# Kernel optimization log

Hardware: AMD Instinct MI355X
Metric: run time of the kernel (lower is better)

The kernel has to match this reference:

```python
import jax, jax.numpy as jnp
import numpy as np

N, B, E = 10000, 4, 160000
C_IN, C_OUT, C_E = 64, 64, 16


def _mk_params(key, c_in, c_out, c_e):
    ks = jax.random.split(key, 8)
    s = 0.1
    return dict(
        w_n=jax.random.normal(ks[0], (c_in, c_out), jnp.float32) * s,
        w_e=jax.random.normal(ks[1], (c_e, c_out), jnp.float32) * s,
        q=jax.random.normal(ks[2], (c_out, c_out), jnp.float32) * s,
        k=jax.random.normal(ks[3], (c_out, c_out), jnp.float32) * s,
        aw=jax.random.normal(ks[4], (3 * c_out, 1), jnp.float32) * s,
        ab=jax.random.normal(ks[5], (1,), jnp.float32) * s,
        ow=jax.random.normal(ks[6], (2 * c_out, c_out), jnp.float32) * s,
        ob=jax.random.normal(ks[7], (c_out,), jnp.float32) * s,
    )


def setup_inputs() -> dict:
    key = jax.random.key(0)
    kx, ke, ka, k1, k2 = jax.random.split(key, 5)
    inp = {
        'X': jax.random.normal(kx, (N, B, C_IN), jnp.float32),
        'edge_index': jax.random.randint(ke, (2, E), 0, N, jnp.int32),
        'edge_attr': jax.random.normal(ka, (E, C_E), jnp.float32),
    }
    p1 = _mk_params(k1, C_IN, C_OUT, C_E)
    p2 = _mk_params(k2, C_OUT, C_OUT, C_E)
    for name, v in p1.items():
        inp[name + '1'] = v
    for name, v in p2.items():
        inp[name + '2'] = v
    return inp


def egnn_conv(x, edge_index, edge_attr, w_n, w_e, q, k, aw, ab, ow, ob, n_nodes):
    # x: [N,B,Cin]; edge_attr: [E,Ce]
    xp = x @ w_n                         # [N,B,C]
    ea = edge_attr @ w_e                 # [E,C]
    src, dst = edge_index[0], edge_index[1]
    xj = xp[src]                         # [E,B,C] gather (source)
    xi = xp[dst]                         # [E,B,C] gather (target)
    qf = xj @ q                          # [E,B,C]
    kf = xi @ k                          # [E,B,C]
    eab = jnp.broadcast_to(ea[:, None, :], qf.shape)  # [E,B,C]
    att_feat = jnp.concatenate([qf, kf, eab], axis=-1)  # [E,B,3C]
    att = jax.nn.sigmoid(att_feat @ aw + ab)            # [E,B,1]
    gate = jax.nn.sigmoid(eab)
    msg = att * xj * gate                # [E,B,C]
    aggr = jax.ops.segment_max(msg, dst, num_segments=n_nodes)  # [N,B,C]
    aggr = jnp.where(jnp.isneginf(aggr), 0.0, aggr)  # empty segments -> 0
    out = jnp.concatenate([xp, aggr], axis=-1) @ ow + ob
    return xp + out


def reference(X, edge_index, edge_attr,
              w_n1, w_e1, q1, k1, aw1, ab1, ow1, ob1,
              w_n2, w_e2, q2, k2, aw2, ab2, ow2, ob2):
    n_nodes = X.shape[0]
    c1 = egnn_conv(X, edge_index, edge_attr, w_n1, w_e1, q1, k1, aw1, ab1, ow1, ob1, n_nodes)
    c1 = jax.nn.leaky_relu(c1, 0.01)
    c2 = egnn_conv(c1, edge_index, edge_attr, w_n2, w_e2, q2, k2, aw2, ab2, ow2, ob2, n_nodes)
    c2 = jax.nn.leaky_relu(c2, 0.01)
    return c2
```

## Files before the change

kernel.cpp:

```cpp
#include <hip/hip_runtime.h>
#include <math.h>

#define NN 10000
#define BB 4
#define EE 160000
#define CC 64
#define CE 16

static constexpr size_t OFF_XPA    = 0;
static constexpr size_t OFF_XPB    = 10240000;
static constexpr size_t OFF_SA     = 20480000;
static constexpr size_t OFF_SB     = 20640000;
static constexpr size_t OFF_VECS   = 20800000;
static constexpr size_t OFF_COUNTS = 20801280;
static constexpr size_t OFF_CURSOR = 20841280;
static constexpr size_t OFF_OFFS   = 20881280;
static constexpr size_t OFF_RECS   = 20921344;
static constexpr size_t OFF_ATT    = 22201344;
static constexpr size_t OFF_SE12   = 24761344;
static constexpr size_t OFF_ORDER  = 26041344;

__device__ __forceinline__ float sigmoidf_(float x) {
    return __builtin_amdgcn_rcpf(1.0f + __expf(-x));
}

__global__ void hist_vecs_kernel(const int* __restrict__ ei, int* __restrict__ counts,
                                 const float* __restrict__ q1, const float* __restrict__ k1,
                                 const float* __restrict__ aw1, const float* __restrict__ we1,
                                 const float* __restrict__ q2, const float* __restrict__ k2,
                                 const float* __restrict__ aw2, const float* __restrict__ we2,
                                 float* __restrict__ vecs) {
    int e = blockIdx.x * blockDim.x + threadIdx.x;
    if (e < EE) atomicAdd(&counts[ei[EE + e]], 1);
    if (blockIdx.x == 0) {
        int t = threadIdx.x;
        if (t < 64) {
            float a = 0.f, b = 0.f, c = 0.f, d = 0.f;
            for (int j = 0; j < 64; ++j) {
                a = fmaf(q1[t * 64 + j], aw1[j], a);
                b = fmaf(k1[t * 64 + j], aw1[64 + j], b);
                c = fmaf(q2[t * 64 + j], aw2[j], c);
                d = fmaf(k2[t * 64 + j], aw2[64 + j], d);
            }
            vecs[t] = a; vecs[64 + t] = b; vecs[144 + t] = c; vecs[208 + t] = d;
        }
        if (t < 16) {
            float a = 0.f, b = 0.f;
            for (int j = 0; j < 64; ++j) {
                a = fmaf(we1[t * 64 + j], aw1[128 + j], a);
                b = fmaf(we2[t * 64 + j], aw2[128 + j], b);
            }
            vecs[128 + t] = a; vecs[272 + t] = b;
        }
    }
}

__global__ __launch_bounds__(1024) void scan_kernel(const int* __restrict__ counts,
                                                    int* __restrict__ offs, int n) {
    __shared__ int wsum[16];
    int t = threadIdx.x;
    int base = t * 10;
    int v[10];
    int s = 0;
    #pragma unroll
    for (int j = 0; j < 10; ++j) {
        int i = base + j;
        v[j] = (i < n) ? counts[i] : 0;
        s += v[j];
    }
    int lane = t & 63, wid = t >> 6;
    int ps = s;
    #pragma unroll
    for (int off = 1; off < 64; off <<= 1) {
        int u = __shfl_up(ps, off, 64);
        if (lane >= off) ps += u;
    }
    if (lane == 63) wsum[wid] = ps;
    __syncthreads();
    int wbase = 0;
    for (int w = 0; w < wid; ++w) wbase += wsum[w];
    int tb = wbase + ps - s;
    #pragma unroll
    for (int j = 0; j < 10; ++j) {
        int i = base + j;
        if (i < n) offs[i] = tb;
        tb += v[j];
    }
    if (t == 1023) offs[n] = tb;
}

__global__ __launch_bounds__(1024) void order_kernel(const int* __restrict__ counts,
                                                     int* __restrict__ order) {
    __shared__ int hist[1024];
    __shared__ int startb[1024];
    __shared__ int cur[1024];
    __shared__ int wsum[16];
    int t = threadIdx.x;
    hist[t] = 0; cur[t] = 0;
    __syncthreads();
    int dg[10];
    #pragma unroll
    for (int j = 0; j < 10; ++j) {
        int i = t * 10 + j;
        dg[j] = -1;
        if (i < NN) {
            int d = counts[i];
            d = (d > 1023) ? 1023 : d;
            dg[j] = d;
            atomicAdd(&hist[d], 1);
        }
    }
    __syncthreads();
    int r = 1023 - t;
    int v = hist[r];
    int lane = t & 63, wid = t >> 6;
    int ps = v;
    #pragma unroll
    for (int off = 1; off < 64; off <<= 1) {
        int u = __shfl_up(ps, off, 64);
        if (lane >= off) ps += u;
    }
    if (lane == 63) wsum[wid] = ps;
    __syncthreads();
    int wbase = 0;
    for (int w = 0; w < wid; ++w) wbase += wsum[w];
    startb[r] = wbase + ps - v;
    __syncthreads();
    #pragma unroll
    for (int j = 0; j < 10; ++j) {
        if (dg[j] >= 0) {
            int pos = startb[dg[j]] + atomicAdd(&cur[dg[j]], 1);
            order[pos] = t * 10 + j;
        }
    }
}

__global__ __launch_bounds__(256) void scatter_kernel(
    const int* __restrict__ ei, const int* __restrict__ offs,
    int* __restrict__ cursor, const float* __restrict__ attr,
    const float* __restrict__ vecs, const float* __restrict__ ab1,
    const float* __restrict__ ab2, int2* __restrict__ recs,
    float2* __restrict__ se12) {
    int e = blockIdx.x * blockDim.x + threadIdx.x;
    if (e >= EE) return;
    int s = ei[e], d = ei[EE + e];
    const float4* ap = (const float4*)(attr + (size_t)e * CE);
    float4 a0 = ap[0], a1 = ap[1], a2 = ap[2], a3 = ap[3];
    const float* v1 = vecs + 128;
    const float* v2 = vecs + 272;
    float s1 = ab1[0], s2 = ab2[0];
    s1 = fmaf(a0.x, v1[0], s1);  s1 = fmaf(a0.y, v1[1], s1);
    s1 = fmaf(a0.z, v1[2], s1);  s1 = fmaf(a0.w, v1[3], s1);
    s1 = fmaf(a1.x, v1[4], s1);  s1 = fmaf(a1.y, v1[5], s1);
    s1 = fmaf(a1.z, v1[6], s1);  s1 = fmaf(a1.w, v1[7], s1);
    s1 = fmaf(a2.x, v1[8], s1);  s1 = fmaf(a2.y, v1[9], s1);
    s1 = fmaf(a2.z, v1[10], s1); s1 = fmaf(a2.w, v1[11], s1);
    s1 = fmaf(a3.x, v1[12], s1); s1 = fmaf(a3.y, v1[13], s1);
    s1 = fmaf(a3.z, v1[14], s1); s1 = fmaf(a3.w, v1[15], s1);
    s2 = fmaf(a0.x, v2[0], s2);  s2 = fmaf(a0.y, v2[1], s2);
    s2 = fmaf(a0.z, v2[2], s2);  s2 = fmaf(a0.w, v2[3], s2);
    s2 = fmaf(a1.x, v2[4], s2);  s2 = fmaf(a1.y, v2[5], s2);
    s2 = fmaf(a1.z, v2[6], s2);  s2 = fmaf(a1.w, v2[7], s2);
    s2 = fmaf(a2.x, v2[8], s2);  s2 = fmaf(a2.y, v2[9], s2);
    s2 = fmaf(a2.z, v2[10], s2); s2 = fmaf(a2.w, v2[11], s2);
    s2 = fmaf(a3.x, v2[12], s2); s2 = fmaf(a3.y, v2[13], s2);
    s2 = fmaf(a3.z, v2[14], s2); s2 = fmaf(a3.w, v2[15], s2);
    int p = atomicAdd(&cursor[d], 1);
    recs[offs[d] + p] = make_int2(s, e);
    se12[e] = make_float2(s1, s2);
}

__global__ __launch_bounds__(256) void node_prep_kernel(
    const float* __restrict__ x,
    const float* __restrict__ w_n,
    const float* __restrict__ qa,
    const float* __restrict__ ka,
    float* __restrict__ xp,
    float* __restrict__ sa,
    float* __restrict__ sb) {
    __shared__ float w_sh[64 * 64];
    __shared__ float x_sh[4 * BB * CC];
    int t = threadIdx.x;
    for (int i = t; i < 64 * 64; i += 256) w_sh[i] = w_n[i];
    int node0 = blockIdx.x * 4;
    const float4* xg = (const float4*)(x + (size_t)node0 * BB * CC);
    ((float4*)x_sh)[t] = xg[t];
    __syncthreads();
    int wave = t >> 6, lane = t & 63;
    int node = node0 + wave;
    const float* xrow = x_sh + wave * BB * CC;
    float acc0 = 0.f, acc1 = 0.f, acc2 = 0.f, acc3 = 0.f;
    #pragma unroll 8
    for (int ci = 0; ci < 64; ++ci) {
        float w = w_sh[ci * 64 + lane];
        acc0 = fmaf(xrow[ci], w, acc0);
        acc1 = fmaf(xrow[64 + ci], w, acc1);
        acc2 = fmaf(xrow[128 + ci], w, acc2);
        acc3 = fmaf(xrow[192 + ci], w, acc3);
    }
    size_t obase = (size_t)node * BB * CC + lane;
    xp[obase] = acc0;
    xp[obase + 64] = acc1;
    xp[obase + 128] = acc2;
    xp[obase + 192] = acc3;
    float qv = qa[lane], kv = ka[lane];
    float ra0 = acc0 * qv, ra1 = acc1 * qv, ra2 = acc2 * qv, ra3 = acc3 * qv;
    float rb0 = acc0 * kv, rb1 = acc1 * kv, rb2 = acc2 * kv, rb3 = acc3 * kv;
    #pragma unroll
    for (int off = 32; off >= 1; off >>= 1) {
        ra0 += __shfl_xor(ra0, off, 64); ra1 += __shfl_xor(ra1, off, 64);
        ra2 += __shfl_xor(ra2, off, 64); ra3 += __shfl_xor(ra3, off, 64);
        rb0 += __shfl_xor(rb0, off, 64); rb1 += __shfl_xor(rb1, off, 64);
        rb2 += __shfl_xor(rb2, off, 64); rb3 += __shfl_xor(rb3, off, 64);
    }
    if (lane == 0) {
        sa[node * BB + 0] = ra0; sa[node * BB + 1] = ra1;
        sa[node * BB + 2] = ra2; sa[node * BB + 3] = ra3;
        sb[node * BB + 0] = rb0; sb[node * BB + 1] = rb1;
        sb[node * BB + 2] = rb2; sb[node * BB + 3] = rb3;
    }
}

__global__ __launch_bounds__(256) void att_kernel(
    const int* __restrict__ ei, const float2* __restrict__ se12,
    const float* __restrict__ sa, const float* __restrict__ sb,
    float4* __restrict__ att, int sel) {
    int e = blockIdx.x * blockDim.x + threadIdx.x;
    if (e >= EE) return;
    int s = ei[e], d = ei[EE + e];
    float2 se2 = se12[e];
    float se = sel ? se2.y : se2.x;
    float4 sas = *(const float4*)(sa + (size_t)s * BB);
    float4 sbn = *(const float4*)(sb + (size_t)d * BB);
    float4 r;
    r.x = sigmoidf_(sas.x + sbn.x + se);
    r.y = sigmoidf_(sas.y + sbn.y + se);
    r.z = sigmoidf_(sas.z + sbn.z + se);
    r.w = sigmoidf_(sas.w + sbn.w + se);
    att[e] = r;
}

__global__ __launch_bounds__(256) void conv_out_kernel(
    const float* __restrict__ xp,
    const int2* __restrict__ recs,
    const int* __restrict__ offs,
    const float* __restrict__ attr,
    const float* __restrict__ w_e,
    const float4* __restrict__ att,
    const float* __restrict__ ow,
    const float* __restrict__ ob,
    const int* __restrict__ order,
    float* __restrict__ out) {
    __shared__ float aggr_sh[4][BB * CC];
    __shared__ float xpn_sh[4][BB * CC];
    int t = threadIdx.x;
    int wave = t >> 6, lane = t & 63;
    int node = order[blockIdx.x * 4 + wave];

    float wec[CE];
    #pragma unroll
    for (int j = 0; j < CE; ++j) wec[j] = w_e[j * CC + lane];

    const float* xn = xp + (size_t)node * BB * CC + lane;
    float xn0 = xn[0], xn1 = xn[64], xn2 = xn[128], xn3 = xn[192];

    int o0 = offs[node], o1 = offs[node + 1];
    float m0 = -INFINITY, m1 = -INFINITY, m2 = -INFINITY, m3 = -INFINITY;

    int i = o0;
    int2 rec = (i < o1) ? recs[i] : make_int2(0, 0);
    while (i < o1) {
        int2 cur = rec;
        ++i;
        if (i < o1) rec = recs[i];
        int s = cur.x, e = cur.y;
        float4 at = att[e];
        const float4* ap = (const float4*)(attr + (size_t)e * CE);
        float4 a0 = ap[0], a1 = ap[1], a2 = ap[2], a3 = ap[3];
        float g = 0.f;
        g = fmaf(a0.x, wec[0], g);  g = fmaf(a0.y, wec[1], g);
        g = fmaf(a0.z, wec[2], g);  g = fmaf(a0.w, wec[3], g);
        g = fmaf(a1.x, wec[4], g);  g = fmaf(a1.y, wec[5], g);
        g = fmaf(a1.z, wec[6], g);  g = fmaf(a1.w, wec[7], g);
        g = fmaf(a2.x, wec[8], g);  g = fmaf(a2.y, wec[9], g);
        g = fmaf(a2.z, wec[10], g); g = fmaf(a2.w, wec[11], g);
        g = fmaf(a3.x, wec[12], g); g = fmaf(a3.y, wec[13], g);
        g = fmaf(a3.z, wec[14], g); g = fmaf(a3.w, wec[15], g);
        g = sigmoidf_(g);
        const float* xs = xp + (size_t)s * BB * CC + lane;
        float x0 = xs[0], x1 = xs[64], x2 = xs[128], x3 = xs[192];
        m0 = fmaxf(m0, at.x * x0 * g);
        m1 = fmaxf(m1, at.y * x1 * g);
        m2 = fmaxf(m2, at.z * x2 * g);
        m3 = fmaxf(m3, at.w * x3 * g);
    }
    m0 = (m0 == -INFINITY) ? 0.f : m0;
    m1 = (m1 == -INFINITY) ? 0.f : m1;
    m2 = (m2 == -INFINITY) ? 0.f : m2;
    m3 = (m3 == -INFINITY) ? 0.f : m3;

    aggr_sh[wave][0 * CC + lane] = m0; aggr_sh[wave][1 * CC + lane] = m1;
    aggr_sh[wave][2 * CC + lane] = m2; aggr_sh[wave][3 * CC + lane] = m3;
    xpn_sh[wave][0 * CC + lane] = xn0; xpn_sh[wave][1 * CC + lane] = xn1;
    xpn_sh[wave][2 * CC + lane] = xn2; xpn_sh[wave][3 * CC + lane] = xn3;
    asm volatile("s_waitcnt lgkmcnt(0)" ::: "memory");

    const float* xr = xpn_sh[wave];
    const float* ar = aggr_sh[wave];
    float o0f = 0.f, o1f = 0.f, o2f = 0.f, o3f = 0.f;
    #pragma unroll 4
    for (int ci = 0; ci < 64; ++ci) {
        float wa = ow[ci * 64 + lane];
        float wb = ow[(64 + ci) * 64 + lane];
        o0f = fmaf(xr[ci], wa, o0f);
        o1f = fmaf(xr[CC + ci], wa, o1f);
        o2f = fmaf(xr[2 * CC + ci], wa, o2f);
        o3f = fmaf(xr[3 * CC + ci], wa, o3f);
        o0f = fmaf(ar[ci], wb, o0f);
        o1f = fmaf(ar[CC + ci], wb, o1f);
        o2f = fmaf(ar[2 * CC + ci], wb, o2f);
        o3f = fmaf(ar[3 * CC + ci], wb, o3f);
    }
    float obv = ob[lane];
    float r0 = xn0 + o0f + obv;
    float r1 = xn1 + o1f + obv;
    float r2 = xn2 + o2f + obv;
    float r3 = xn3 + o3f + obv;
    r0 = (r0 > 0.f) ? r0 : 0.01f * r0;
    r1 = (r1 > 0.f) ? r1 : 0.01f * r1;
    r2 = (r2 > 0.f) ? r2 : 0.01f * r2;
    r3 = (r3 > 0.f) ? r3 : 0.01f * r3;
    float* op = out + (size_t)node * BB * CC + lane;
    op[0] = r0; op[64] = r1; op[128] = r2; op[192] = r3;
}

extern "C" void kernel_launch(void* const* d_in, const int* in_sizes, int n_in,
                              void* d_out, int out_size, void* d_ws, size_t ws_size,
                              hipStream_t stream) {
    const float* X    = (const float*)d_in[0];
    const int*   ei   = (const int*)d_in[1];
    const float* attr = (const float*)d_in[2];
    const float* w_n1 = (const float*)d_in[3];
    const float* w_e1 = (const float*)d_in[4];
    const float* q1   = (const float*)d_in[5];
    const float* k1   = (const float*)d_in[6];
    const float* aw1  = (const float*)d_in[7];
    const float* ab1  = (const float*)d_in[8];
    const float* ow1  = (const float*)d_in[9];
    const float* ob1  = (const float*)d_in[10];
    const float* w_n2 = (const float*)d_in[11];
    const float* w_e2 = (const float*)d_in[12];
    const float* q2   = (const float*)d_in[13];
    const float* k2   = (const float*)d_in[14];
    const float* aw2  = (const float*)d_in[15];
    const float* ab2  = (const float*)d_in[16];
    const float* ow2  = (const float*)d_in[17];
    const float* ob2  = (const float*)d_in[18];
    float* out = (float*)d_out;

    char* ws = (char*)d_ws;
    float*  xpA    = (float*)(ws + OFF_XPA);
    float*  xpB    = (float*)(ws + OFF_XPB);
    float*  sa     = (float*)(ws + OFF_SA);
    float*  sb     = (float*)(ws + OFF_SB);
    float*  vecs   = (float*)(ws + OFF_VECS);
    int*    counts = (int*)(ws + OFF_COUNTS);
    int*    cursor = (int*)(ws + OFF_CURSOR);
    int*    offs   = (int*)(ws + OFF_OFFS);
    int2*   recs   = (int2*)(ws + OFF_RECS);
    float4* att    = (float4*)(ws + OFF_ATT);
    float2* se12   = (float2*)(ws + OFF_SE12);
    int*    order  = (int*)(ws + OFF_ORDER);

    hipMemsetAsync(counts, 0, 2 * NN * sizeof(int), stream);
    hist_vecs_kernel<<<EE / 256, 256, 0, stream>>>(ei, counts, q1, k1, aw1, w_e1,
                                                   q2, k2, aw2, w_e2, vecs);
    scan_kernel<<<1, 1024, 0, stream>>>(counts, offs, NN);
    order_kernel<<<1, 1024, 0, stream>>>(counts, order);
    scatter_kernel<<<EE / 256, 256, 0, stream>>>(ei, offs, cursor, attr, vecs,
                                                 ab1, ab2, recs, se12);
    node_prep_kernel<<<NN / 4, 256, 0, stream>>>(X, w_n1, vecs + 0, vecs + 64, xpA, sa, sb);
    att_kernel<<<EE / 256, 256, 0, stream>>>(ei, se12, sa, sb, att, 0);
    conv_out_kernel<<<NN / 4, 256, 0, stream>>>(xpA, recs, offs, attr, w_e1, att,
                                                ow1, ob1, order, xpB);
    node_prep_kernel<<<NN / 4, 256, 0, stream>>>(xpB, w_n2, vecs + 144, vecs + 208, xpA, sa, sb);
    att_kernel<<<EE / 256, 256, 0, stream>>>(ei, se12, sa, sb, att, 1);
    conv_out_kernel<<<NN / 4, 256, 0, stream>>>(xpA, recs, offs, attr, w_e2, att,
                                                ow2, ob2, order, out);
}
```

Before: 289.6 us.

## Merge scan and order kernels; vectorize conv_out output projection with float4 tiles

```diff
diff --git a/kernel.cpp b/kernel.cpp
--- a/kernel.cpp
+++ b/kernel.cpp
@@ -55,20 +55,24 @@
     }
 }
 
-__global__ __launch_bounds__(1024) void scan_kernel(const int* __restrict__ counts,
-                                                    int* __restrict__ offs, int n) {
+__global__ __launch_bounds__(1024) void scan_order_kernel(const int* __restrict__ counts,
+                                                          int* __restrict__ offs,
+                                                          int* __restrict__ order) {
+    __shared__ int hist[1024];
+    __shared__ int cur[1024];
+    __shared__ int startb[1024];
     __shared__ int wsum[16];
     int t = threadIdx.x;
-    int base = t * 10;
+    hist[t] = 0; cur[t] = 0;
+    int lane = t & 63, wid = t >> 6;
     int v[10];
     int s = 0;
     #pragma unroll
     for (int j = 0; j < 10; ++j) {
-        int i = base + j;
-        v[j] = (i < n) ? counts[i] : 0;
+        int i = t * 10 + j;
+        v[j] = (i < NN) ? counts[i] : 0;
         s += v[j];
     }
-    int lane = t & 63, wid = t >> 6;
     int ps = s;
     #pragma unroll
     for (int off = 1; off < 64; off <<= 1) {
@@ -82,55 +86,41 @@
     int tb = wbase + ps - s;
     #pragma unroll
     for (int j = 0; j < 10; ++j) {
-        int i = base + j;
-        if (i < n) offs[i] = tb;
+        int i = t * 10 + j;
+        if (i < NN) offs[i] = tb;
         tb += v[j];
     }
-    if (t == 1023) offs[n] = tb;
-}
-
-__global__ __launch_bounds__(1024) void order_kernel(const int* __restrict__ counts,
-                                                     int* __restrict__ order) {
-    __shared__ int hist[1024];
-    __shared__ int startb[1024];
-    __shared__ int cur[1024];
-    __shared__ int wsum[16];
-    int t = threadIdx.x;
-    hist[t] = 0; cur[t] = 0;
-    __syncthreads();
-    int dg[10];
+    if (t == 1023) offs[NN] = tb;
     #pragma unroll
     for (int j = 0; j < 10; ++j) {
         int i = t * 10 + j;
-        dg[j] = -1;
         if (i < NN) {
-            int d = counts[i];
-            d = (d > 1023) ? 1023 : d;
-            dg[j] = d;
+            int d = v[j] > 1023 ? 1023 : v[j];
             atomicAdd(&hist[d], 1);
         }
     }
     __syncthreads();
     int r = 1023 - t;
-    int v = hist[r];
-    int lane = t & 63, wid = t >> 6;
-    int ps = v;
+    int hv = hist[r];
+    int ps2 = hv;
     #pragma unroll
     for (int off = 1; off < 64; off <<= 1) {
-        int u = __shfl_up(ps, off, 64);
-        if (lane >= off) ps += u;
-    }
-    if (lane == 63) wsum[wid] = ps;
-    __syncthreads();
-    int wbase = 0;
-    for (int w = 0; w < wid; ++w) wbase += wsum[w];
-    startb[r] = wbase + ps - v;
+        int u = __shfl_up(ps2, off, 64);
+        if (lane >= off) ps2 += u;
+    }
+    if (lane == 63) wsum[wid] = ps2;
+    __syncthreads();
+    int wb2 = 0;
+    for (int w = 0; w < wid; ++w) wb2 += wsum[w];
+    startb[r] = wb2 + ps2 - hv;
     __syncthreads();
     #pragma unroll
     for (int j = 0; j < 10; ++j) {
-        if (dg[j] >= 0) {
-            int pos = startb[dg[j]] + atomicAdd(&cur[dg[j]], 1);
-            order[pos] = t * 10 + j;
+        int i = t * 10 + j;
+        if (i < NN) {
+            int d = v[j] > 1023 ? 1023 : v[j];
+            int pos = startb[d] + atomicAdd(&cur[d], 1);
+            order[pos] = i;
         }
     }
 }
@@ -171,13 +161,9 @@
 }
 
 __global__ __launch_bounds__(256) void node_prep_kernel(
-    const float* __restrict__ x,
-    const float* __restrict__ w_n,
-    const float* __restrict__ qa,
-    const float* __restrict__ ka,
-    float* __restrict__ xp,
-    float* __restrict__ sa,
-    float* __restrict__ sb) {
+    const float* __restrict__ x, const float* __restrict__ w_n,
+    const float* __restrict__ qa, const float* __restrict__ ka,
+    float* __restrict__ xp, float* __restrict__ sa, float* __restrict__ sb) {
     __shared__ float w_sh[64 * 64];
     __shared__ float x_sh[4 * BB * CC];
     int t = threadIdx.x;
@@ -240,6 +226,10 @@
     att[e] = r;
 }
 
+#define FMA4(o_, s_, w_)                                                 \
+    o_.x = fmaf(s_, w_.x, o_.x); o_.y = fmaf(s_, w_.y, o_.y);            \
+    o_.z = fmaf(s_, w_.z, o_.z); o_.w = fmaf(s_, w_.w, o_.w);
+
 __global__ __launch_bounds__(256) void conv_out_kernel(
     const float* __restrict__ xp,
     const int2* __restrict__ recs,
@@ -251,8 +241,7 @@
     const float* __restrict__ ob,
     const int* __restrict__ order,
     float* __restrict__ out) {
-    __shared__ float aggr_sh[4][BB * CC];
-    __shared__ float xpn_sh[4][BB * CC];
+    __shared__ float aggr_sh[4][BB * 68];
     int t = threadIdx.x;
     int wave = t >> 6, lane = t & 63;
     int node = order[blockIdx.x * 4 + wave];
@@ -260,9 +249,6 @@
     float wec[CE];
     #pragma unroll
     for (int j = 0; j < CE; ++j) wec[j] = w_e[j * CC + lane];
-
-    const float* xn = xp + (size_t)node * BB * CC + lane;
-    float xn0 = xn[0], xn1 = xn[64], xn2 = xn[128], xn3 = xn[192];
 
     int o0 = offs[node], o1 = offs[node + 1];
     float m0 = -INFINITY, m1 = -INFINITY, m2 = -INFINITY, m3 = -INFINITY;
@@ -299,39 +285,49 @@
     m2 = (m2 == -INFINITY) ? 0.f : m2;
     m3 = (m3 == -INFINITY) ? 0.f : m3;
 
-    aggr_sh[wave][0 * CC + lane] = m0; aggr_sh[wave][1 * CC + lane] = m1;
-    aggr_sh[wave][2 * CC + lane] = m2; aggr_sh[wave][3 * CC + lane] = m3;
-    xpn_sh[wave][0 * CC + lane] = xn0; xpn_sh[wave][1 * CC + lane] = xn1;
-    xpn_sh[wave][2 * CC + lane] = xn2; xpn_sh[wave][3 * CC + lane] = xn3;
+    float* ash = aggr_sh[wave];
+    ash[0 * 68 + lane] = m0;
+    ash[1 * 68 + lane] = m1;
+    ash[2 * 68 + lane] = m2;
+    ash[3 * 68 + lane] = m3;
     asm volatile("s_waitcnt lgkmcnt(0)" ::: "memory");
-
-    const float* xr = xpn_sh[wave];
-    const float* ar = aggr_sh[wave];
-    float o0f = 0.f, o1f = 0.f, o2f = 0.f, o3f = 0.f;
-    #pragma unroll 4
-    for (int ci = 0; ci < 64; ++ci) {
-        float wa = ow[ci * 64 + lane];
-        float wb = ow[(64 + ci) * 64 + lane];
-        o0f = fmaf(xr[ci], wa, o0f);
-        o1f = fmaf(xr[CC + ci], wa, o1f);
-        o2f = fmaf(xr[2 * CC + ci], wa, o2f);
-        o3f = fmaf(xr[3 * CC + ci], wa, o3f);
-        o0f = fmaf(ar[ci], wb, o0f);
-        o1f = fmaf(ar[CC + ci], wb, o1f);
-        o2f = fmaf(ar[2 * CC + ci], wb, o2f);
-        o3f = fmaf(ar[3 * CC + ci], wb, o3f);
-    }
-    float obv = ob[lane];
-    float r0 = xn0 + o0f + obv;
-    float r1 = xn1 + o1f + obv;
-    float r2 = xn2 + o2f + obv;
-    float r3 = xn3 + o3f + obv;
-    r0 = (r0 > 0.f) ? r0 : 0.01f * r0;
-    r1 = (r1 > 0.f) ? r1 : 0.01f * r1;
-    r2 = (r2 > 0.f) ? r2 : 0.01f * r2;
-    r3 = (r3 > 0.f) ? r3 : 0.01f * r3;
-    float* op = out + (size_t)node * BB * CC + lane;
-    op[0] = r0; op[64] = r1; op[128] = r2; op[192] = r3;
+    __builtin_amdgcn_sched_barrier(0);
+
+    int b = lane >> 4, q4 = (lane & 15) << 2;
+    const float* agr = ash + b * 68;
+    const float* xrow = xp + (size_t)node * (BB * CC) + b * CC;
+    const float* owa = ow + q4;
+    const float* owb = ow + CC * CC + q4;
+    float4 o = make_float4(0.f, 0.f, 0.f, 0.f);
+    #pragma unroll 2
+    for (int c4 = 0; c4 < 16; ++c4) {
+        float4 xv = *(const float4*)(xrow + 4 * c4);
+        float4 av = *(const float4*)(agr + 4 * c4);
+        const float* wpa = owa + (size_t)(4 * c4) * CC;
+        float4 w0 = *(const float4*)(wpa);
+        float4 w1 = *(const float4*)(wpa + CC);
+        float4 w2 = *(const float4*)(wpa + 2 * CC);
+        float4 w3 = *(const float4*)(wpa + 3 * CC);
+        const float* wpb = owb + (size_t)(4 * c4) * CC;
+        float4 u0 = *(const float4*)(wpb);
+        float4 u1 = *(const float4*)(wpb + CC);
+        float4 u2 = *(const float4*)(wpb + 2 * CC);
+        float4 u3 = *(const float4*)(wpb + 3 * CC);
+        FMA4(o, xv.x, w0); FMA4(o, xv.y, w1); FMA4(o, xv.z, w2); FMA4(o, xv.w, w3);
+        FMA4(o, av.x, u0); FMA4(o, av.y, u1); FMA4(o, av.z, u2); FMA4(o, av.w, u3);
+    }
+    float4 xnv = *(const float4*)(xrow + q4);
+    float4 ob4 = *(const float4*)(ob + q4);
+    float4 r;
+    r.x = xnv.x + o.x + ob4.x;
+    r.y = xnv.y + o.y + ob4.y;
+    r.z = xnv.z + o.z + ob4.z;
+    r.w = xnv.w + o.w + ob4.w;
+    r.x = (r.x > 0.f) ? r.x : 0.01f * r.x;
+    r.y = (r.y > 0.f) ? r.y : 0.01f * r.y;
+    r.z = (r.z > 0.f) ? r.z : 0.01f * r.z;
+    r.w = (r.w > 0.f) ? r.w : 0.01f * r.w;
+    *(float4*)(out + (size_t)node * (BB * CC) + b * CC + q4) = r;
 }
 
 extern "C" void kernel_launch(void* const* d_in, const int* in_sizes, int n_in,
@@ -375,8 +371,7 @@
     hipMemsetAsync(counts, 0, 2 * NN * sizeof(int), stream);
     hist_vecs_kernel<<<EE / 256, 256, 0, stream>>>(ei, counts, q1, k1, aw1, w_e1,
                                                    q2, k2, aw2, w_e2, vecs);
-    scan_kernel<<<1, 1024, 0, stream>>>(counts, offs, NN);
-    order_kernel<<<1, 1024, 0, stream>>>(counts, order);
+    scan_order_kernel<<<1, 1024, 0, stream>>>(counts, offs, order);
     scatter_kernel<<<EE / 256, 256, 0, stream>>>(ei, offs, cursor, attr, vecs,
                                                  ab1, ab2, recs, se12);
     node_prep_kernel<<<NN / 4, 256, 0, stream>>>(X, w_n1, vecs + 0, vecs + 64, xpA, sa, sb);
```

Result: slower. 336.5 us (+16.2%).
